# Kernel tuning notes

Measured on AMD Instinct MI355X. Metric: run time of the kernel, lower is better.

The kernel has to match this reference:

```python
import jax, jax.numpy as jnp
import numpy as np

B, T, H, NIN, D = 128, 64, 100, 3, 10


def _gru_cell(x, h, Wih, Whh, bih, bhh):
    # torch GRU cell: r,z,n gate ordering
    gi = x @ Wih.T + bih
    gh = h @ Whh.T + bhh
    ir, iz, inn = jnp.split(gi, 3, axis=-1)
    hr, hz, hn = jnp.split(gh, 3, axis=-1)
    r = jax.nn.sigmoid(ir + hr)
    z = jax.nn.sigmoid(iz + hz)
    n = jnp.tanh(inn + r * hn)
    return (1.0 - z) * n + z * h


def setup_inputs():
    keys = iter(jax.random.split(jax.random.key(0), 64))
    def rn(shape, scale):
        return jax.random.normal(next(keys), shape, dtype=jnp.float32) * scale
    inp = {"received": jax.random.normal(next(keys), (B, T, NIN), dtype=jnp.float32)}
    s = float(1.0 / np.sqrt(H))
    for p in ("w1", "w2"):
        inp[p + "_ih0"] = rn((3 * H, NIN), s)
        inp[p + "_hh0"] = rn((3 * H, H), s)
        inp[p + "_bih0"] = rn((3 * H,), s)
        inp[p + "_bhh0"] = rn((3 * H,), s)
        inp[p + "_ih1"] = rn((3 * H, H), s)
        inp[p + "_hh1"] = rn((3 * H, H), s)
        inp[p + "_bih1"] = rn((3 * H,), s)
        inp[p + "_bhh1"] = rn((3 * H,), s)
    s2 = float(1.0 / np.sqrt(2 * H))
    inp["attn_w"] = rn((1, 2 * H), s2)
    inp["attn_b"] = rn((1,), s2)
    inp["ctx_w"] = rn((H, 2 * H), s2)
    inp["ctx_b"] = rn((H,), s2)
    inp["out_w"] = rn((1, 2 * H), s2)
    inp["out_b"] = rn((1,), s2)
    return inp


def _forward(received, P1, P2, attn_w, attn_b, ctx_w, ctx_b, out_w, out_b):
    def two_layer(x, h, P):
        ih0, hh0, bih0, bhh0, ih1, hh1, bih1, bhh1 = P
        h0 = _gru_cell(x, h[0], ih0, hh0, bih0, bhh0)
        h1 = _gru_cell(h0, h[1], ih1, hh1, bih1, bhh1)
        # out = top-layer hidden; new hidden state [2,B,H]
        return h1, jnp.stack([h0, h1])

    def attend(hn, cache, t):
        # hn [2,B,H] (raw GRU hidden), cache [2,B,T,H] of past raw hiddens
        hrep = jnp.broadcast_to(hn[:, :, None, :], cache.shape)
        e = (jnp.concatenate([hrep, cache], axis=-1) @ attn_w.T)[..., 0] + attn_b[0]  # [2,B,T]
        mask = jnp.arange(T) < jnp.maximum(t, 1)  # safe mask (never all-False)
        a = jax.nn.softmax(jnp.where(mask, e, -1e30), axis=-1)
        c = jnp.einsum('lbt,lbth->lbh', a, cache)
        return jnp.concatenate([c, hn], axis=-1) @ ctx_w.T + ctx_b

    x_tm = jnp.transpose(received, (1, 0, 2))  # [T,B,NIN]
    h_init = jnp.zeros((2, B, H), jnp.float32)
    cache_init = jnp.zeros((2, B, T, H), jnp.float32)

    def step(carry, inp):
        h1, h2, c1, c2 = carry
        x, t = inp
        o1, h1n = two_layer(x, h1, P1)
        o2, h2n = two_layer(x, h2, P2)
        # attention over hiddens from steps 0..t-1 (cache updated AFTER attending)
        h1mix = attend(h1n, c1, t)
        h2mix = attend(h2n, c2, t)
        c1 = jax.lax.dynamic_update_slice(c1, h1n[:, :, None, :], (0, 0, t, 0))
        c2 = jax.lax.dynamic_update_slice(c2, h2n[:, :, None, :], (0, 0, t, 0))
        first = (t == 0)
        h1next = jnp.where(first, h1n, h1mix)
        h2next = jnp.where(first, h2n, h2mix)
        return (h1next, h2next, c1, c2), (o1, o2)

    _, (out1, out2) = jax.lax.scan(step, (h_init, h_init, cache_init, cache_init),
                                   (x_tm, jnp.arange(T)))
    out1 = jnp.transpose(out1, (1, 0, 2))  # [B,T,H]
    out2 = jnp.transpose(out2, (1, 0, 2))
    # readout: bit i pairs rnn_out1[i] with rnn_out2[min(i+D, T-1)]
    idx = jnp.minimum(jnp.arange(T) + D, T - 1)
    rnn_out = jnp.concatenate([out1, out2[:, idx, :]], axis=-1)  # [B,T,2H]
    logits = rnn_out @ out_w.T + out_b  # dec_act == 'linear'
    return jax.nn.sigmoid(logits)  # [B,T,1]


def reference(received, w1_ih0, w1_hh0, w1_bih0, w1_bhh0, w1_ih1, w1_hh1, w1_bih1, w1_bhh1,
              w2_ih0, w2_hh0, w2_bih0, w2_bhh0, w2_ih1, w2_hh1, w2_bih1, w2_bhh1,
              attn_w, attn_b, ctx_w, ctx_b, out_w, out_b):
    P1 = (w1_ih0, w1_hh0, w1_bih0, w1_bhh0, w1_ih1, w1_hh1, w1_bih1, w1_bhh1)
    P2 = (w2_ih0, w2_hh0, w2_bih0, w2_bhh0, w2_ih1, w2_hh1, w2_bih1, w2_bhh1)
    return _forward(received, P1, P2, attn_w, attn_b, ctx_w, ctx_b, out_w, out_b)
```

## Files before the change

kernel.cpp:

```cpp
#include <hip/hip_runtime.h>
#include <stdint.h>

#define H100 100
#define T64  64
#define NB   128
#define DLAG 10

#define OFF_HH0 0
#define OFF_IH1 30000
#define OFF_HH1 60000
#define OFF_CTX 90000
#define OFF_AWC 100000
#define OFF_OW  100050
#define OFF_P   100152

typedef _Float16 half2_t __attribute__((ext_vector_type(2)));
typedef __fp16   pk16x2  __attribute__((ext_vector_type(2)));

__device__ __forceinline__ float fdot2u(uint32_t a, uint32_t b, float c) {
#if __has_builtin(__builtin_amdgcn_fdot2)
    return __builtin_amdgcn_fdot2(__builtin_bit_cast(half2_t, a),
                                  __builtin_bit_cast(half2_t, b), c, false);
#else
    half2_t ha = __builtin_bit_cast(half2_t, a), hb = __builtin_bit_cast(half2_t, b);
    return c + (float)ha[0]*(float)hb[0] + (float)ha[1]*(float)hb[1];
#endif
}
__device__ __forceinline__ uint32_t pkrtz(float a, float b) {
    pk16x2 h = __builtin_amdgcn_cvt_pkrtz(a, b);
    return __builtin_bit_cast(uint32_t, h);
}
__device__ __forceinline__ uint32_t pk_rn(float a, float b) {
    half2_t h; h[0] = (_Float16)a; h[1] = (_Float16)b;
    return __builtin_bit_cast(uint32_t, h);
}
__device__ __forceinline__ float lo16(uint32_t u){ return (float)__builtin_bit_cast(half2_t,u)[0]; }
__device__ __forceinline__ float hi16(uint32_t u){ return (float)__builtin_bit_cast(half2_t,u)[1]; }
__device__ __forceinline__ float sigm(float x){ return 1.f/(1.f+__expf(-x)); }
__device__ __forceinline__ float tanhfast(float x){ return 1.f - 2.f/(1.f+__expf(2.f*x)); }
__device__ __forceinline__ float gru_el(float pr, float pz, float gin, float ghn, float hp) {
    float r = sigm(pr), z = sigm(pz);
    float n = tanhfast(gin + r*ghn);
    return (1.f - z)*n + z*hp;
}
__device__ __forceinline__ float wsum(float v){
    #pragma unroll
    for (int off = 32; off; off >>= 1) v += __shfl_xor(v, off);
    return v;
}
__device__ __forceinline__ float wmax(float v){
    #pragma unroll
    for (int off = 32; off; off >>= 1) v = fmaxf(v, __shfl_xor(v, off));
    return v;
}
__device__ __forceinline__ uint32_t rlane(uint32_t v, int lane){
    return (uint32_t)__builtin_amdgcn_readlane((int)v, lane);
}

struct SMem {
    alignas(16) uint32_t cache_t[2][50][66];
    alignas(16) float grz1[200];
    alignas(16) float gin1[100];
    alignas(16) float ghn1[100];
    alignas(16) float grz2[200];
    alignas(16) float gin2[100];
    alignas(16) float ghn2[100];
    alignas(16) float sv[2][64];
    alignas(16) float atile[2][64];
    alignas(16) uint32_t cpkq[2][64];
    alignas(16) float hmix0[104];
    alignas(16) float hmix1[104];
    alignas(16) float x[192];
};

__global__ void prep_pack(const float* __restrict__ w1hh0, const float* __restrict__ w2hh0,
                          const float* __restrict__ w1ih1, const float* __restrict__ w2ih1,
                          const float* __restrict__ w1hh1, const float* __restrict__ w2hh1,
                          const float* __restrict__ attw,  const float* __restrict__ ctxw,
                          const float* __restrict__ outw,  uint32_t* __restrict__ ws) {
    int g = blockIdx.x*blockDim.x + threadIdx.x;
    if (g < 30000) {
        int br = g/15000, idx = g%15000;
        int j = idx/50, kp = idx%50;
        const float* w = br ? w2hh0 : w1hh0;
        ws[OFF_HH0 + g] = pk_rn(w[j*H100+2*kp], w[j*H100+2*kp+1]);
    } else if (g < 60000) {
        int t2 = g-30000; int br = t2/15000, idx = t2%15000;
        int j = idx/50, kp = idx%50;
        const float* w = br ? w2ih1 : w1ih1;
        ws[OFF_IH1 + t2] = pk_rn(w[j*H100+2*kp], w[j*H100+2*kp+1]);
    } else if (g < 90000) {
        int t2 = g-60000; int br = t2/15000, idx = t2%15000;
        int j = idx/50, kp = idx%50;
        const float* w = br ? w2hh1 : w1hh1;
        ws[OFF_HH1 + t2] = pk_rn(w[j*H100+2*kp], w[j*H100+2*kp+1]);
    } else if (g < 100000) {
        int idx = g-90000; int o = idx/100, kp = idx%100;
        ws[OFF_CTX + idx] = pk_rn(ctxw[o*200+2*kp], ctxw[o*200+2*kp+1]);
    } else if (g < 100050) {
        int i2 = g-100000;
        ws[OFF_AWC + i2] = pk_rn(attw[100+2*i2], attw[101+2*i2]);
    } else if (g < 100150) {
        int t2 = g-100050; int br = t2/50, i2 = t2%50;
        ws[OFF_OW + t2] = pk_rn(outw[br*H100+2*i2], outw[br*H100+2*i2+1]);
    }
}

__global__ __launch_bounds__(512, 1)
void gru_seq(const float* __restrict__ recv,
             const float* __restrict__ ih0_1, const float* __restrict__ bih0_1,
             const float* __restrict__ bhh0_1, const float* __restrict__ bih1_1,
             const float* __restrict__ bhh1_1,
             const float* __restrict__ ih0_2, const float* __restrict__ bih0_2,
             const float* __restrict__ bhh0_2, const float* __restrict__ bih1_2,
             const float* __restrict__ bhh1_2,
             const float* __restrict__ ctxb,
             uint32_t* __restrict__ ws) {
    __shared__ SMem S;
    const int tid = threadIdx.x;
    const int w   = tid >> 6;
    const int la  = tid & 63;
    const int br  = blockIdx.x >> 7;
    const int b   = blockIdx.x & 127;

    const float* ih0 = br ? ih0_2  : ih0_1;
    const float* bi0 = br ? bih0_2 : bih0_1;
    const float* bh0 = br ? bhh0_2 : bhh0_1;
    const float* bi1 = br ? bih1_2 : bih1_1;
    const float* bh1 = br ? bhh1_2 : bhh1_1;

    for (int i = tid; i < 192; i += 512) S.x[i] = recv[b*192 + i];
    for (int i = tid; i < 2*50*66; i += 512) ((uint32_t*)S.cache_t)[i] = 0u;
    if (tid < 128) S.sv[tid>>6][tid&63] = 0.f;

    uint32_t wA[50], wB[50], wC[50];
    float fb0=0.f, fb1=0.f, fb2=0.f, fb3=0.f;
    float rix0=0.f, rix1=0.f, rix2=0.f;
    if (tid < 300) {
        const uint32_t* p0 = ws + OFF_HH0 + br*15000 + tid*50;
        const uint32_t* p1 = ws + OFF_HH1 + br*15000 + tid*50;
        const uint32_t* p2 = ws + OFF_IH1 + br*15000 + tid*50;
        #pragma unroll
        for (int k = 0; k < 50; ++k) { wA[k] = p0[k]; wB[k] = p1[k]; wC[k] = p2[k]; }
        fb0 = bi0[tid]; fb1 = bh0[tid]; fb2 = bi1[tid]; fb3 = bh1[tid];
        rix0 = ih0[tid*3]; rix1 = ih0[tid*3+1]; rix2 = ih0[tid*3+2];
    } else if (tid < 400) {
        const int o = tid - 300;
        const uint32_t* pc = ws + OFF_CTX + o*100;
        #pragma unroll
        for (int k = 0; k < 50; ++k) { wA[k] = pc[k]; wB[k] = pc[50+k]; }
        fb0 = ctxb[o];
    }
    uint32_t rawc = 0u, rowp = 0u;
    if (w == 0 && la < 50) rawc = ws[OFF_AWC + la];
    if (w == 7 && la < 50) rowp = ws[OFF_OW + br*50 + la];
    float* p_out = (float*)(ws + OFF_P);

    uint32_t hn0p = 0u, hn1p = 0u, h0cp = 0u, h1cp = 0u;
    float gh1save = 0.f;
    __syncthreads();

    for (int t = 0; t < T64; ++t) {
        if (la < 50) {
            if (t == 0)      { h0cp = 0u;   h1cp = 0u;   }
            else if (t == 1) { h0cp = hn0p; h1cp = hn1p; }
            else {
                float2 a0 = *(const float2*)&S.hmix0[2*la];
                float2 a1 = *(const float2*)&S.hmix1[2*la];
                h0cp = pkrtz(a0.x, a0.y);
                h1cp = pkrtz(a1.x, a1.y);
            }
        }
        if (tid < 300) {
            float x0 = S.x[3*t], x1 = S.x[3*t+1], x2 = S.x[3*t+2];
            float accI = fb0 + rix0*x0 + rix1*x1 + rix2*x2;
            float a0=0.f,a1=0.f,a2=0.f,a3=0.f, b0=0.f,b1=0.f,b2=0.f,b3=0.f;
            #pragma unroll
            for (int k = 0; k < 48; k += 4) {
                uint32_t h0a=rlane(h0cp,k), h0b=rlane(h0cp,k+1), h0c=rlane(h0cp,k+2), h0d=rlane(h0cp,k+3);
                uint32_t h1a=rlane(h1cp,k), h1b=rlane(h1cp,k+1), h1c=rlane(h1cp,k+2), h1d=rlane(h1cp,k+3);
                a0 = fdot2u(wA[k],   h0a, a0);
                b0 = fdot2u(wB[k],   h1a, b0);
                a1 = fdot2u(wA[k+1], h0b, a1);
                b1 = fdot2u(wB[k+1], h1b, b1);
                a2 = fdot2u(wA[k+2], h0c, a2);
                b2 = fdot2u(wB[k+2], h1c, b2);
                a3 = fdot2u(wA[k+3], h0d, a3);
                b3 = fdot2u(wB[k+3], h1d, b3);
            }
            {
                uint32_t h0a=rlane(h0cp,48), h0b=rlane(h0cp,49);
                uint32_t h1a=rlane(h1cp,48), h1b=rlane(h1cp,49);
                a0 = fdot2u(wA[48], h0a, a0);
                b0 = fdot2u(wB[48], h1a, b0);
                a1 = fdot2u(wA[49], h0b, a1);
                b1 = fdot2u(wB[49], h1b, b1);
            }
            float acc0 = fb1 + ((a0+a1)+(a2+a3));
            gh1save    = fb3 + ((b0+b1)+(b2+b3));
            if (tid < 200) S.grz1[tid] = accI + acc0;
            else { S.gin1[tid-200] = accI; S.ghn1[tid-200] = acc0; }
        } else if (w == 5 || w == 6) {
            const int l = w - 5;
            const int m = (t > 1) ? t : 1;
            float sval = S.sv[l][la];
            float sv2  = (la < m) ? sval : -3e38f;
            float mx   = wmax(sv2);
            float p    = (la < m) ? __expf(sv2 - mx) : 0.f;
            float ssum = wsum(p);
            S.atile[l][la] = p;
            if (la < 50) {
                float c0 = 0.f, c1 = 0.f;
                const uint32_t* crow = &S.cache_t[l][la][0];
                const int np = (m + 1) >> 1;
                for (int tp = 0; tp < np; ++tp) {
                    float2 ap = *(const float2*)&S.atile[l][2*tp];
                    uint2  cp = *(const uint2*)&crow[2*tp];
                    c0 += ap.x*lo16(cp.x) + ap.y*lo16(cp.y);
                    c1 += ap.x*hi16(cp.x) + ap.y*hi16(cp.y);
                }
                float inv = 1.f/ssum;
                S.cpkq[l][la] = pkrtz(c0*inv, c1*inv);
            }
        } else if (w == 7 && t > 0) {
            float v = (la < 50) ? fdot2u(rowp, hn1p, 0.f) : 0.f;
            v = wsum(v);
            if (la == 0) p_out[br*8192 + b*64 + (t-1)] = v;
        }
        __syncthreads();
        if (la < 50) {
            float2 pr = *(const float2*)&S.grz1[2*la];
            float2 pz = *(const float2*)&S.grz1[100+2*la];
            float2 gi = *(const float2*)&S.gin1[2*la];
            float2 gh = *(const float2*)&S.ghn1[2*la];
            float h0 = gru_el(pr.x, pz.x, gi.x, gh.x, lo16(h0cp));
            float h1 = gru_el(pr.y, pz.y, gi.y, gh.y, hi16(h0cp));
            hn0p = pkrtz(h0, h1);
        }
        if (w == 0) {
            float v = (la < 50) ? fdot2u(rawc, hn0p, 0.f) : 0.f;
            v = wsum(v);
            if (la == 0) S.sv[0][t] = v;
            if (la < 50) S.cache_t[0][la][t] = hn0p;
        }
        if (tid < 300) {
            float g0=0.f,g1=0.f,g2=0.f,g3=0.f;
            #pragma unroll
            for (int k = 0; k < 48; k += 4) {
                uint32_t ha=rlane(hn0p,k), hb=rlane(hn0p,k+1), hc=rlane(hn0p,k+2), hd=rlane(hn0p,k+3);
                g0 = fdot2u(wC[k],   ha, g0);
                g1 = fdot2u(wC[k+1], hb, g1);
                g2 = fdot2u(wC[k+2], hc, g2);
                g3 = fdot2u(wC[k+3], hd, g3);
            }
            {
                uint32_t ha=rlane(hn0p,48), hb=rlane(hn0p,49);
                g0 = fdot2u(wC[48], ha, g0);
                g1 = fdot2u(wC[49], hb, g1);
            }
            float gi1 = fb2 + ((g0+g1)+(g2+g3));
            if (tid < 200) S.grz2[tid] = gi1 + gh1save;
            else { S.gin2[tid-200] = gi1; S.ghn2[tid-200] = gh1save; }
        }
        __syncthreads();
        if (la < 50) {
            float2 pr = *(const float2*)&S.grz2[2*la];
            float2 pz = *(const float2*)&S.grz2[100+2*la];
            float2 gi = *(const float2*)&S.gin2[2*la];
            float2 gh = *(const float2*)&S.ghn2[2*la];
            float h0 = gru_el(pr.x, pz.x, gi.x, gh.x, lo16(h1cp));
            float h1 = gru_el(pr.y, pz.y, gi.y, gh.y, hi16(h1cp));
            hn1p = pkrtz(h0, h1);
        }
        if (w == 0) {
            float v = (la < 50) ? fdot2u(rawc, hn1p, 0.f) : 0.f;
            v = wsum(v);
            if (la == 0) S.sv[1][t] = v;
            if (la < 50) S.cache_t[1][la][t] = hn1p;
        }
        if (tid >= 300 && tid < 400) {
            float p0a=fb0, p0b=0.f, p1a=fb0, p1b=0.f;
            #pragma unroll
            for (int k = 0; k < 50; k += 2) {
                uint2 v0 = *(const uint2*)&S.cpkq[0][k];
                uint2 v1 = *(const uint2*)&S.cpkq[1][k];
                p0a = fdot2u(wA[k],   v0.x, p0a);
                p1a = fdot2u(wA[k],   v1.x, p1a);
                p0b = fdot2u(wA[k+1], v0.y, p0b);
                p1b = fdot2u(wA[k+1], v1.y, p1b);
            }
            float q0a=0.f, q0b=0.f, q1a=0.f, q1b=0.f;
            #pragma unroll
            for (int k = 0; k < 50; k += 2) {
                uint32_t ha=rlane(hn0p,k), hb=rlane(hn0p,k+1);
                uint32_t hc=rlane(hn1p,k), hd=rlane(hn1p,k+1);
                q0a = fdot2u(wB[k],   ha, q0a);
                q1a = fdot2u(wB[k],   hc, q1a);
                q0b = fdot2u(wB[k+1], hb, q0b);
                q1b = fdot2u(wB[k+1], hd, q1b);
            }
            S.hmix0[tid-300] = (p0a+p0b) + (q0a+q0b);
            S.hmix1[tid-300] = (p1a+p1b) + (q1a+q1b);
        }
        __syncthreads();
    }
    if (w == 7) {
        float v = (la < 50) ? fdot2u(rowp, hn1p, 0.f) : 0.f;
        v = wsum(v);
        if (la == 0) p_out[br*8192 + b*64 + 63] = v;
    }
}

__global__ void fin_out(const uint32_t* __restrict__ ws, const float* __restrict__ outb,
                        float* __restrict__ out) {
    int i = blockIdx.x*blockDim.x + threadIdx.x;
    if (i >= NB*T64) return;
    int b = i >> 6, t = i & 63;
    const float* p = (const float*)(ws + OFF_P);
    int t2 = t + DLAG; if (t2 > T64-1) t2 = T64-1;
    float logit = p[0*8192 + b*64 + t] + p[1*8192 + b*64 + t2] + outb[0];
    out[i] = 1.f/(1.f+__expf(-logit));
}

extern "C" void kernel_launch(void* const* d_in, const int* in_sizes, int n_in,
                              void* d_out, int out_size, void* d_ws, size_t ws_size,
                              hipStream_t stream) {
    const float* recv   = (const float*)d_in[0];
    const float* w1ih0  = (const float*)d_in[1];
    const float* w1hh0  = (const float*)d_in[2];
    const float* w1bih0 = (const float*)d_in[3];
    const float* w1bhh0 = (const float*)d_in[4];
    const float* w1ih1  = (const float*)d_in[5];
    const float* w1hh1  = (const float*)d_in[6];
    const float* w1bih1 = (const float*)d_in[7];
    const float* w1bhh1 = (const float*)d_in[8];
    const float* w2ih0  = (const float*)d_in[9];
    const float* w2hh0  = (const float*)d_in[10];
    const float* w2bih0 = (const float*)d_in[11];
    const float* w2bhh0 = (const float*)d_in[12];
    const float* w2ih1  = (const float*)d_in[13];
    const float* w2hh1  = (const float*)d_in[14];
    const float* w2bih1 = (const float*)d_in[15];
    const float* w2bhh1 = (const float*)d_in[16];
    const float* attw   = (const float*)d_in[17];
    const float* ctxw   = (const float*)d_in[19];
    const float* ctxb   = (const float*)d_in[20];
    const float* outw   = (const float*)d_in[21];
    const float* outb   = (const float*)d_in[22];
    uint32_t* ws = (uint32_t*)d_ws;
    float* out = (float*)d_out;

    prep_pack<<<(100150 + 255)/256, 256, 0, stream>>>(
        w1hh0, w2hh0, w1ih1, w2ih1, w1hh1, w2hh1, attw, ctxw, outw, ws);

    gru_seq<<<256, 512, 0, stream>>>(
        recv,
        w1ih0, w1bih0, w1bhh0, w1bih1, w1bhh1,
        w2ih0, w2bih0, w2bhh0, w2bih1, w2bhh1,
        ctxb, ws);

    fin_out<<<(NB*T64 + 255)/256, 256, 0, stream>>>(ws, outb, out);
}
```

Baseline: 240.6 us.

## Split context projection across 200 threads and move attention scores to idle wave

The context projection for the two layers was done by 100 threads, each computing both layers. It is now spread over 200 threads, one output per layer each, which halves the serial dot-product chain per thread. The attention-score and cache-write work moves from wave 0, which also computes gates, to wave 7, which is otherwise idle. The attention reduction loop is unrolled by 8 with batched LDS loads. These shorten the critical path of each timestep. The cost is more threads holding weight registers and extra branching.

```diff
diff --git a/kernel.cpp b/kernel.cpp
--- a/kernel.cpp
+++ b/kernel.cpp
@@ -60,14 +60,14 @@
 struct SMem {
     alignas(16) uint32_t cache_t[2][50][66];
     alignas(16) float grz1[200];
-    alignas(16) float gin1[100];
-    alignas(16) float ghn1[100];
+    alignas(16) float gin1[104];
+    alignas(16) float ghn1[104];
     alignas(16) float grz2[200];
-    alignas(16) float gin2[100];
-    alignas(16) float ghn2[100];
+    alignas(16) float gin2[104];
+    alignas(16) float ghn2[104];
     alignas(16) float sv[2][64];
     alignas(16) float atile[2][64];
-    alignas(16) uint32_t cpkq[2][64];
+    alignas(16) uint32_t cpkq[2][52];
     alignas(16) float hmix0[104];
     alignas(16) float hmix1[104];
     alignas(16) float x[192];
@@ -132,28 +132,31 @@
     for (int i = tid; i < 192; i += 512) S.x[i] = recv[b*192 + i];
     for (int i = tid; i < 2*50*66; i += 512) ((uint32_t*)S.cache_t)[i] = 0u;
     if (tid < 128) S.sv[tid>>6][tid&63] = 0.f;
-
-    uint32_t wA[50], wB[50], wC[50];
+    if (tid < 104) { S.cpkq[0][tid>>1] = 0u; S.cpkq[1][tid>>1] = 0u; }
+
+    uint32_t wreg[150];
     float fb0=0.f, fb1=0.f, fb2=0.f, fb3=0.f;
     float rix0=0.f, rix1=0.f, rix2=0.f;
+    int cl=0, co=0;
     if (tid < 300) {
         const uint32_t* p0 = ws + OFF_HH0 + br*15000 + tid*50;
         const uint32_t* p1 = ws + OFF_HH1 + br*15000 + tid*50;
         const uint32_t* p2 = ws + OFF_IH1 + br*15000 + tid*50;
         #pragma unroll
-        for (int k = 0; k < 50; ++k) { wA[k] = p0[k]; wB[k] = p1[k]; wC[k] = p2[k]; }
+        for (int k = 0; k < 50; ++k) { wreg[k] = p0[k]; wreg[50+k] = p1[k]; wreg[100+k] = p2[k]; }
         fb0 = bi0[tid]; fb1 = bh0[tid]; fb2 = bi1[tid]; fb3 = bh1[tid];
         rix0 = ih0[tid*3]; rix1 = ih0[tid*3+1]; rix2 = ih0[tid*3+2];
-    } else if (tid < 400) {
-        const int o = tid - 300;
-        const uint32_t* pc = ws + OFF_CTX + o*100;
+    } else if (tid < 500) {
+        const int idx = tid - 300;
+        cl = (idx >= 100) ? 1 : 0;
+        co = idx - cl*100;
+        const uint32_t* pc = ws + OFF_CTX + co*100;
         #pragma unroll
-        for (int k = 0; k < 50; ++k) { wA[k] = pc[k]; wB[k] = pc[50+k]; }
-        fb0 = ctxb[o];
+        for (int k = 0; k < 100; ++k) wreg[k] = pc[k];
+        fb0 = ctxb[co];
     }
     uint32_t rawc = 0u, rowp = 0u;
-    if (w == 0 && la < 50) rawc = ws[OFF_AWC + la];
-    if (w == 7 && la < 50) rowp = ws[OFF_OW + br*50 + la];
+    if (w == 7 && la < 50) { rawc = ws[OFF_AWC + la]; rowp = ws[OFF_OW + br*50 + la]; }
     float* p_out = (float*)(ws + OFF_P);
 
     uint32_t hn0p = 0u, hn1p = 0u, h0cp = 0u, h1cp = 0u;
@@ -171,6 +174,11 @@
                 h1cp = pkrtz(a1.x, a1.y);
             }
         }
+        if (w == 7 && t > 0) {
+            float v = (la < 50) ? fdot2u(rowp, hn1p, 0.f) : 0.f;
+            v = wsum(v);
+            if (la == 0) p_out[br*8192 + b*64 + (t-1)] = v;
+        }
         if (tid < 300) {
             float x0 = S.x[3*t], x1 = S.x[3*t+1], x2 = S.x[3*t+2];
             float accI = fb0 + rix0*x0 + rix1*x1 + rix2*x2;
@@ -179,22 +187,22 @@
             for (int k = 0; k < 48; k += 4) {
                 uint32_t h0a=rlane(h0cp,k), h0b=rlane(h0cp,k+1), h0c=rlane(h0cp,k+2), h0d=rlane(h0cp,k+3);
                 uint32_t h1a=rlane(h1cp,k), h1b=rlane(h1cp,k+1), h1c=rlane(h1cp,k+2), h1d=rlane(h1cp,k+3);
-                a0 = fdot2u(wA[k],   h0a, a0);
-                b0 = fdot2u(wB[k],   h1a, b0);
-                a1 = fdot2u(wA[k+1], h0b, a1);
-                b1 = fdot2u(wB[k+1], h1b, b1);
-                a2 = fdot2u(wA[k+2], h0c, a2);
-                b2 = fdot2u(wB[k+2], h1c, b2);
-                a3 = fdot2u(wA[k+3], h0d, a3);
-                b3 = fdot2u(wB[k+3], h1d, b3);
+                a0 = fdot2u(wreg[k],   h0a, a0);
+                b0 = fdot2u(wreg[50+k],h1a, b0);
+                a1 = fdot2u(wreg[k+1],   h0b, a1);
+                b1 = fdot2u(wreg[50+k+1],h1b, b1);
+                a2 = fdot2u(wreg[k+2],   h0c, a2);
+                b2 = fdot2u(wreg[50+k+2],h1c, b2);
+                a3 = fdot2u(wreg[k+3],   h0d, a3);
+                b3 = fdot2u(wreg[50+k+3],h1d, b3);
             }
             {
                 uint32_t h0a=rlane(h0cp,48), h0b=rlane(h0cp,49);
                 uint32_t h1a=rlane(h1cp,48), h1b=rlane(h1cp,49);
-                a0 = fdot2u(wA[48], h0a, a0);
-                b0 = fdot2u(wB[48], h1a, b0);
-                a1 = fdot2u(wA[49], h0b, a1);
-                b1 = fdot2u(wB[49], h1b, b1);
+                a0 = fdot2u(wreg[48], h0a, a0);
+                b0 = fdot2u(wreg[98], h1a, b0);
+                a1 = fdot2u(wreg[49], h0b, a1);
+                b1 = fdot2u(wreg[99], h1b, b1);
             }
             float acc0 = fb1 + ((a0+a1)+(a2+a3));
             gh1save    = fb3 + ((b0+b1)+(b2+b3));
@@ -213,19 +221,22 @@
                 float c0 = 0.f, c1 = 0.f;
                 const uint32_t* crow = &S.cache_t[l][la][0];
                 const int np = (m + 1) >> 1;
-                for (int tp = 0; tp < np; ++tp) {
-                    float2 ap = *(const float2*)&S.atile[l][2*tp];
-                    uint2  cp = *(const uint2*)&crow[2*tp];
-                    c0 += ap.x*lo16(cp.x) + ap.y*lo16(cp.y);
-                    c1 += ap.x*hi16(cp.x) + ap.y*hi16(cp.y);
+                for (int tb = 0; tb < np; tb += 8) {
+                    float2 ap[8]; uint2 cp[8];
+                    #pragma unroll
+                    for (int j = 0; j < 8; ++j) {
+                        ap[j] = *(const float2*)&S.atile[l][2*(tb+j)];
+                        cp[j] = *(const uint2*)&crow[2*(tb+j)];
+                    }
+                    #pragma unroll
+                    for (int j = 0; j < 8; ++j) {
+                        c0 += ap[j].x*lo16(cp[j].x) + ap[j].y*lo16(cp[j].y);
+                        c1 += ap[j].x*hi16(cp[j].x) + ap[j].y*hi16(cp[j].y);
+                    }
                 }
                 float inv = 1.f/ssum;
                 S.cpkq[l][la] = pkrtz(c0*inv, c1*inv);
             }
-        } else if (w == 7 && t > 0) {
-            float v = (la < 50) ? fdot2u(rowp, hn1p, 0.f) : 0.f;
-            v = wsum(v);
-            if (la == 0) p_out[br*8192 + b*64 + (t-1)] = v;
         }
         __syncthreads();
         if (la < 50) {
@@ -237,30 +248,29 @@
             float h1 = gru_el(pr.y, pz.y, gi.y, gh.y, hi16(h0cp));
             hn0p = pkrtz(h0, h1);
         }
-        if (w == 0) {
-            float v = (la < 50) ? fdot2u(rawc, hn0p, 0.f) : 0.f;
-            v = wsum(v);
-            if (la == 0) S.sv[0][t] = v;
-            if (la < 50) S.cache_t[0][la][t] = hn0p;
-        }
         if (tid < 300) {
             float g0=0.f,g1=0.f,g2=0.f,g3=0.f;
             #pragma unroll
             for (int k = 0; k < 48; k += 4) {
                 uint32_t ha=rlane(hn0p,k), hb=rlane(hn0p,k+1), hc=rlane(hn0p,k+2), hd=rlane(hn0p,k+3);
-                g0 = fdot2u(wC[k],   ha, g0);
-                g1 = fdot2u(wC[k+1], hb, g1);
-                g2 = fdot2u(wC[k+2], hc, g2);
-                g3 = fdot2u(wC[k+3], hd, g3);
+                g0 = fdot2u(wreg[100+k],   ha, g0);
+                g1 = fdot2u(wreg[100+k+1], hb, g1);
+                g2 = fdot2u(wreg[100+k+2], hc, g2);
+                g3 = fdot2u(wreg[100+k+3], hd, g3);
             }
             {
                 uint32_t ha=rlane(hn0p,48), hb=rlane(hn0p,49);
-                g0 = fdot2u(wC[48], ha, g0);
-                g1 = fdot2u(wC[49], hb, g1);
+                g0 = fdot2u(wreg[148], ha, g0);
+                g1 = fdot2u(wreg[149], hb, g1);
             }
             float gi1 = fb2 + ((g0+g1)+(g2+g3));
             if (tid < 200) S.grz2[tid] = gi1 + gh1save;
             else { S.gin2[tid-200] = gi1; S.ghn2[tid-200] = gh1save; }
+        } else if (w == 7) {
+            if (la < 50) S.cache_t[0][la][t] = hn0p;
+            float v = (la < 50) ? fdot2u(rawc, hn0p, 0.f) : 0.f;
+            v = wsum(v);
+            if (la == 0) S.sv[0][t] = v;
         }
         __syncthreads();
         if (la < 50) {
@@ -272,35 +282,55 @@
             float h1 = gru_el(pr.y, pz.y, gi.y, gh.y, hi16(h1cp));
             hn1p = pkrtz(h0, h1);
         }
-        if (w == 0) {
+        if (tid >= 300 && tid < 500) {
+            float p0=fb0, p1=0.f, p2=0.f, p3=0.f;
+            #pragma unroll
+            for (int i = 0; i < 12; ++i) {
+                uint4 c = *(const uint4*)&S.cpkq[cl][4*i];
+                p0 = fdot2u(wreg[4*i],   c.x, p0);
+                p1 = fdot2u(wreg[4*i+1], c.y, p1);
+                p2 = fdot2u(wreg[4*i+2], c.z, p2);
+                p3 = fdot2u(wreg[4*i+3], c.w, p3);
+            }
+            {
+                uint2 c = *(const uint2*)&S.cpkq[cl][48];
+                p0 = fdot2u(wreg[48], c.x, p0);
+                p1 = fdot2u(wreg[49], c.y, p1);
+            }
+            float q0=0.f,q1=0.f,q2=0.f,q3=0.f;
+            if (cl) {
+                #pragma unroll
+                for (int k = 0; k < 48; k += 4) {
+                    uint32_t ha=rlane(hn1p,k), hb=rlane(hn1p,k+1), hc=rlane(hn1p,k+2), hd=rlane(hn1p,k+3);
+                    q0 = fdot2u(wreg[50+k],   ha, q0);
+                    q1 = fdot2u(wreg[50+k+1], hb, q1);
+                    q2 = fdot2u(wreg[50+k+2], hc, q2);
+                    q3 = fdot2u(wreg[50+k+3], hd, q3);
+                }
+                uint32_t ha=rlane(hn1p,48), hb=rlane(hn1p,49);
+                q0 = fdot2u(wreg[98], ha, q0);
+                q1 = fdot2u(wreg[99], hb, q1);
+            } else {
+                #pragma unroll
+                for (int k = 0; k < 48; k += 4) {
+                    uint32_t ha=rlane(hn0p,k), hb=rlane(hn0p,k+1), hc=rlane(hn0p,k+2), hd=rlane(hn0p,k+3);
+                    q0 = fdot2u(wreg[50+k],   ha, q0);
+                    q1 = fdot2u(wreg[50+k+1], hb, q1);
+                    q2 = fdot2u(wreg[50+k+2], hc, q2);
+                    q3 = fdot2u(wreg[50+k+3], hd, q3);
+                }
+                uint32_t ha=rlane(hn0p,48), hb=rlane(hn0p,49);
+                q0 = fdot2u(wreg[98], ha, q0);
+                q1 = fdot2u(wreg[99], hb, q1);
+            }
+            float hm = ((p0+p1)+(p2+p3)) + ((q0+q1)+(q2+q3));
+            if (cl) S.hmix1[co] = hm; else S.hmix0[co] = hm;
+        }
+        if (w == 7) {
+            if (la < 50) S.cache_t[1][la][t] = hn1p;
             float v = (la < 50) ? fdot2u(rawc, hn1p, 0.f) : 0.f;
             v = wsum(v);
             if (la == 0) S.sv[1][t] = v;
-            if (la < 50) S.cache_t[1][la][t] = hn1p;
-        }
-        if (tid >= 300 && tid < 400) {
-            float p0a=fb0, p0b=0.f, p1a=fb0, p1b=0.f;
-            #pragma unroll
-            for (int k = 0; k < 50; k += 2) {
-                uint2 v0 = *(const uint2*)&S.cpkq[0][k];
-                uint2 v1 = *(const uint2*)&S.cpkq[1][k];
-                p0a = fdot2u(wA[k],   v0.x, p0a);
-                p1a = fdot2u(wA[k],   v1.x, p1a);
-                p0b = fdot2u(wA[k+1], v0.y, p0b);
-                p1b = fdot2u(wA[k+1], v1.y, p1b);
-            }
-            float q0a=0.f, q0b=0.f, q1a=0.f, q1b=0.f;
-            #pragma unroll
-            for (int k = 0; k < 50; k += 2) {
-                uint32_t ha=rlane(hn0p,k), hb=rlane(hn0p,k+1);
-                uint32_t hc=rlane(hn1p,k), hd=rlane(hn1p,k+1);
-                q0a = fdot2u(wB[k],   ha, q0a);
-                q1a = fdot2u(wB[k],   hc, q1a);
-                q0b = fdot2u(wB[k+1], hb, q0b);
-                q1b = fdot2u(wB[k+1], hd, q1b);
-            }
-            S.hmix0[tid-300] = (p0a+p0b) + (q0a+q0b);
-            S.hmix1[tid-300] = (p1a+p1b) + (q1a+q1b);
         }
         __syncthreads();
     }
```

Result: no change. 238.4 us (-0.9%).
